# Kernel optimization log

Hardware: AMD Instinct MI355X
Metric: run time of the kernel (lower is better)

Reference implementation:

```python
import jax, jax.numpy as jnp
import numpy as np

B, D, K, L, V = 4096, 512, 10, 256, 80


def setup_inputs() -> dict:
    key = jax.random.key(0)
    k1, k2, k3, k4, k5, k6 = jax.random.split(key, 6)
    inputs = jax.random.normal(k1, (B, D), dtype=jnp.float32)
    prev_kappa = jax.random.uniform(k2, (B, K), dtype=jnp.float32)
    char_ids = jax.random.randint(k3, (B, L), 0, V)
    char_seq_one_hot = jax.nn.one_hot(char_ids, V, dtype=jnp.float32)
    sequence_lengths = jax.random.randint(k4, (B,), 1, L + 1).astype(jnp.int32)
    # Dense params: VarianceScaling(scale=2.0, fan_avg) ~ N(0, 2/((D+3K)/2)) truncated
    std = np.sqrt(2.0 / ((D + 3 * K) / 2.0))
    W = (jax.random.truncated_normal(k5, -2.0, 2.0, (D, 3 * K)) * std).astype(jnp.float32)
    b = jnp.zeros((3 * K,), dtype=jnp.float32)
    kappa_scale = jnp.float32(-2.5)
    return {
        "inputs": inputs,
        "prev_kappa": prev_kappa,
        "char_seq_one_hot": char_seq_one_hot,
        "sequence_lengths": sequence_lengths,
        "W": W,
        "b": b,
        "kappa_scale": kappa_scale,
    }


def reference(inputs, prev_kappa, char_seq_one_hot, sequence_lengths, W, b, kappa_scale):
    raw = inputs @ W + b  # [B, 3K]
    alpha_hat, beta_hat, kappa_hat = jnp.split(raw, 3, axis=1)  # each [B, K]
    alpha = jnp.exp(jnp.clip(alpha_hat, -8.0, 8.0))
    beta = jnp.exp(jnp.clip(beta_hat, -8.0, 8.0))
    delta_kappa = jnp.exp(jnp.clip(kappa_hat + kappa_scale, -8.0, 5.0))
    kappa = prev_kappa + delta_kappa  # [B, K]

    char_len = char_seq_one_hot.shape[1]
    u = jnp.arange(1, char_len + 1, dtype=jnp.float32)  # [L]
    # exponent: [B, K, L]
    exponent = -beta[:, :, None] * jnp.square(kappa[:, :, None] - u[None, None, :])
    exponent = jnp.clip(exponent, -50.0, 0.0)
    phi = jnp.sum(alpha[:, :, None] * jnp.exp(exponent), axis=1)  # [B, L]

    seq_mask = (jnp.arange(char_len)[None, :] < sequence_lengths[:, None]).astype(jnp.float32)
    phi = phi * seq_mask
    phi = jnp.where(jnp.isfinite(phi), phi, 0.0)

    w = jnp.einsum("bl,blv->bv", phi, char_seq_one_hot)  # [B, V]
    w = jnp.where(jnp.isfinite(w), w, 0.0)
    return (w, kappa)
```

## Files before the change

kernel.cpp:

```cpp
#include <hip/hip_runtime.h>

#define B_ 4096
#define D_ 512
#define K_ 10
#define L_ 256
#define V_ 80

__global__ __launch_bounds__(256) void gemv_kernel(
    const float* __restrict__ x,
    const float* __restrict__ prev_kappa,
    const float* __restrict__ W,
    const float* __restrict__ bias,
    const float* __restrict__ kscale,
    float* __restrict__ ws_alpha,
    float* __restrict__ ws_beta,
    float* __restrict__ out_kappa)
{
    const int tid  = threadIdx.x;
    const int wave = tid >> 6;
    const int lane = tid & 63;
    const int r0   = blockIdx.x * 4;
    const int jbase = wave * 8;
    const int jcnt  = (wave == 3) ? 6 : 8;

    const float* xb = x + (size_t)r0 * D_;

    float acc[4][8];
#pragma unroll
    for (int r = 0; r < 4; ++r)
#pragma unroll
        for (int jj = 0; jj < 8; ++jj) acc[r][jj] = 0.f;

#pragma unroll
    for (int i = 0; i < 8; ++i) {
        const int d = lane + 64 * i;
        const float* wrow = W + d * 30 + jbase;
        float wv[8];
#pragma unroll
        for (int jj = 0; jj < 8; ++jj)
            wv[jj] = (jj < 6 || wave < 3) ? wrow[jj] : 0.f;
#pragma unroll
        for (int r = 0; r < 4; ++r) {
            const float xv = xb[r * D_ + d];
#pragma unroll
            for (int jj = 0; jj < 8; ++jj)
                acc[r][jj] = fmaf(xv, wv[jj], acc[r][jj]);
        }
    }

#pragma unroll
    for (int r = 0; r < 4; ++r)
#pragma unroll
        for (int jj = 0; jj < 8; ++jj)
#pragma unroll
            for (int s = 32; s >= 1; s >>= 1)
                acc[r][jj] += __shfl_xor(acc[r][jj], s, 64);

    __shared__ float s_raw[4][30];
    if (lane < jcnt) {
#pragma unroll
        for (int r = 0; r < 4; ++r) {
            float v = acc[r][0];
#pragma unroll
            for (int jj = 1; jj < 8; ++jj) v = (lane == jj) ? acc[r][jj] : v;
            s_raw[r][jbase + lane] = v;
        }
    }
    __syncthreads();

    if (tid < 40) {
        const int r = tid / 10;
        const int k = tid - r * 10;
        const int row = r0 + r;

        const float a_hat = s_raw[r][k]      + bias[k];
        const float b_hat = s_raw[r][10 + k] + bias[10 + k];
        const float k_hat = s_raw[r][20 + k] + bias[20 + k];

        ws_alpha[row * K_ + k] = __expf(fminf(fmaxf(a_hat, -8.f), 8.f));
        ws_beta[row * K_ + k]  = __expf(fminf(fmaxf(b_hat, -8.f), 8.f));
        const float dk = __expf(fminf(fmaxf(k_hat + kscale[0], -8.f), 5.f));
        out_kappa[row * K_ + k] = prev_kappa[row * K_ + k] + dk;
    }
}

__global__ __launch_bounds__(256) void scatter_kernel(
    const float* __restrict__ oh,
    const int*   __restrict__ seqlen,
    const float* __restrict__ ws_alpha,
    const float* __restrict__ ws_beta,
    const float* __restrict__ kappa,
    float* __restrict__ out_w)
{
    const int b   = blockIdx.x;
    const int tid = threadIdx.x;

    __shared__ float s_a[K_], s_b[K_], s_k[K_];
    __shared__ float s_phi[L_];
    __shared__ float s_w[V_];

    if (tid < K_) {
        s_a[tid] = ws_alpha[b * K_ + tid];
        s_b[tid] = ws_beta[b * K_ + tid];
        s_k[tid] = kappa[b * K_ + tid];
    }
    if (tid < V_) s_w[tid] = 0.f;

    const int sl = seqlen[b];
    __syncthreads();

    if (tid < sl) {
        const float u = (float)(tid + 1);
        float phi = 0.f;
#pragma unroll
        for (int k = 0; k < K_; ++k) {
            const float diff = s_k[k] - u;
            float e = fmaxf(-s_b[k] * diff * diff, -50.f);
            phi = fmaf(s_a[k], __expf(e), phi);
        }
        s_phi[tid] = phi;
    }
    __syncthreads();

    const int total4 = sl * (V_ / 4);
    const float4* ohb = (const float4*)(oh + (size_t)b * (L_ * V_));

    for (int f = tid; f < total4; f += 512) {
        const float4 v0 = ohb[f];
        const int f1 = f + 256;
        const bool has1 = (f1 < total4);
        float4 v1 = make_float4(0.f, 0.f, 0.f, 0.f);
        if (has1) v1 = ohb[f1];

        {
            const int l  = f / 20;
            const int vb = (f - l * 20) * 4;
            const float p = s_phi[l];
            if (v0.x != 0.f) atomicAdd(&s_w[vb + 0], p * v0.x);
            if (v0.y != 0.f) atomicAdd(&s_w[vb + 1], p * v0.y);
            if (v0.z != 0.f) atomicAdd(&s_w[vb + 2], p * v0.z);
            if (v0.w != 0.f) atomicAdd(&s_w[vb + 3], p * v0.w);
        }
        if (has1) {
            const int l  = f1 / 20;
            const int vb = (f1 - l * 20) * 4;
            const float p = s_phi[l];
            if (v1.x != 0.f) atomicAdd(&s_w[vb + 0], p * v1.x);
            if (v1.y != 0.f) atomicAdd(&s_w[vb + 1], p * v1.y);
            if (v1.z != 0.f) atomicAdd(&s_w[vb + 2], p * v1.z);
            if (v1.w != 0.f) atomicAdd(&s_w[vb + 3], p * v1.w);
        }
    }
    __syncthreads();

    if (tid < V_) out_w[b * V_ + tid] = s_w[tid];
}

extern "C" void kernel_launch(void* const* d_in, const int* in_sizes, int n_in,
                              void* d_out, int out_size, void* d_ws, size_t ws_size,
                              hipStream_t stream) {
    const float* x          = (const float*)d_in[0];
    const float* prev_kappa = (const float*)d_in[1];
    const float* oh         = (const float*)d_in[2];
    const int*   seqlen     = (const int*)d_in[3];
    const float* W          = (const float*)d_in[4];
    const float* bias       = (const float*)d_in[5];
    const float* kscale     = (const float*)d_in[6];

    float* out   = (float*)d_out;
    float* out_w = out;
    float* out_k = out + B_ * V_;

    float* wsf      = (float*)d_ws;
    float* ws_alpha = wsf;
    float* ws_beta  = wsf + B_ * K_;

    gemv_kernel<<<B_ / 4, 256, 0, stream>>>(x, prev_kappa, W, bias, kscale,
                                            ws_alpha, ws_beta, out_k);
    scatter_kernel<<<B_, 256, 0, stream>>>(oh, seqlen, ws_alpha, ws_beta, out_k,
                                           out_w);
}
```

Baseline: 434.9 us.

## Restructure GEMV via LDS-staged rows and replace atomic scatter with per-column dot reduction

The GEMV kernel now stages 8 input rows in padded shared memory and has each of 240 threads compute one output column with a serial 512-long dot product, replacing the wave-shuffle reduction. The scatter kernel drops shared-memory atomics over float4 one-hot chunks. Instead, 320 threads each own one vocabulary column and one of four row groups, accumulate phi*onehot with strided scalar loads up to a padded sequence length, then reduce the four partials. This removes atomic contention and branchy per-element work, at the cost of uncoalesced-stride reads within a row group and a serial inner loop in the GEMV.

```diff
diff --git a/kernel.cpp b/kernel.cpp
--- a/kernel.cpp
+++ b/kernel.cpp
@@ -5,6 +5,8 @@
 #define K_ 10
 #define L_ 256
 #define V_ 80
+
+#define XSTRIDE 520
 
 __global__ __launch_bounds__(256) void gemv_kernel(
     const float* __restrict__ x,
@@ -16,75 +18,54 @@
     float* __restrict__ ws_beta,
     float* __restrict__ out_kappa)
 {
-    const int tid  = threadIdx.x;
-    const int wave = tid >> 6;
-    const int lane = tid & 63;
-    const int r0   = blockIdx.x * 4;
-    const int jbase = wave * 8;
-    const int jcnt  = (wave == 3) ? 6 : 8;
+    const int tid = threadIdx.x;
+    const int r0  = blockIdx.x * 8;
 
-    const float* xb = x + (size_t)r0 * D_;
+    __shared__ float x_lds[8 * XSTRIDE];
 
-    float acc[4][8];
+    {
+        const float4* xg = (const float4*)(x + (size_t)r0 * D_);
 #pragma unroll
-    for (int r = 0; r < 4; ++r)
-#pragma unroll
-        for (int jj = 0; jj < 8; ++jj) acc[r][jj] = 0.f;
-
-#pragma unroll
-    for (int i = 0; i < 8; ++i) {
-        const int d = lane + 64 * i;
-        const float* wrow = W + d * 30 + jbase;
-        float wv[8];
-#pragma unroll
-        for (int jj = 0; jj < 8; ++jj)
-            wv[jj] = (jj < 6 || wave < 3) ? wrow[jj] : 0.f;
-#pragma unroll
-        for (int r = 0; r < 4; ++r) {
-            const float xv = xb[r * D_ + d];
-#pragma unroll
-            for (int jj = 0; jj < 8; ++jj)
-                acc[r][jj] = fmaf(xv, wv[jj], acc[r][jj]);
-        }
-    }
-
-#pragma unroll
-    for (int r = 0; r < 4; ++r)
-#pragma unroll
-        for (int jj = 0; jj < 8; ++jj)
-#pragma unroll
-            for (int s = 32; s >= 1; s >>= 1)
-                acc[r][jj] += __shfl_xor(acc[r][jj], s, 64);
-
-    __shared__ float s_raw[4][30];
-    if (lane < jcnt) {
-#pragma unroll
-        for (int r = 0; r < 4; ++r) {
-            float v = acc[r][0];
-#pragma unroll
-            for (int jj = 1; jj < 8; ++jj) v = (lane == jj) ? acc[r][jj] : v;
-            s_raw[r][jbase + lane] = v;
+        for (int i = 0; i < 4; ++i) {
+            const int f4 = tid + i * 256;
+            const float4 v = xg[f4];
+            const int f = f4 * 4;
+            const int r = f >> 9;
+            const int c = f & 511;
+            *(float4*)&x_lds[r * XSTRIDE + c] = v;
         }
     }
     __syncthreads();
 
-    if (tid < 40) {
-        const int r = tid / 10;
-        const int k = tid - r * 10;
+    if (tid < 240) {
+        const int r = tid / 30;
+        const int j = tid - r * 30;
         const int row = r0 + r;
+        const float* xr = &x_lds[r * XSTRIDE];
 
-        const float a_hat = s_raw[r][k]      + bias[k];
-        const float b_hat = s_raw[r][10 + k] + bias[10 + k];
-        const float k_hat = s_raw[r][20 + k] + bias[20 + k];
+        float a0 = 0.f, a1 = 0.f, a2 = 0.f, a3 = 0.f;
+#pragma unroll 4
+        for (int d = 0; d < D_; d += 4) {
+            a0 = fmaf(xr[d + 0], W[(d + 0) * 30 + j], a0);
+            a1 = fmaf(xr[d + 1], W[(d + 1) * 30 + j], a1);
+            a2 = fmaf(xr[d + 2], W[(d + 2) * 30 + j], a2);
+            a3 = fmaf(xr[d + 3], W[(d + 3) * 30 + j], a3);
+        }
+        const float v = (a0 + a1) + (a2 + a3) + bias[j];
 
-        ws_alpha[row * K_ + k] = __expf(fminf(fmaxf(a_hat, -8.f), 8.f));
-        ws_beta[row * K_ + k]  = __expf(fminf(fmaxf(b_hat, -8.f), 8.f));
-        const float dk = __expf(fminf(fmaxf(k_hat + kscale[0], -8.f), 5.f));
-        out_kappa[row * K_ + k] = prev_kappa[row * K_ + k] + dk;
+        if (j < 10) {
+            ws_alpha[row * K_ + j] = __expf(fminf(fmaxf(v, -8.f), 8.f));
+        } else if (j < 20) {
+            ws_beta[row * K_ + (j - 10)] = __expf(fminf(fmaxf(v, -8.f), 8.f));
+        } else {
+            const int k = j - 20;
+            const float dk = __expf(fminf(fmaxf(v + kscale[0], -8.f), 5.f));
+            out_kappa[row * K_ + k] = prev_kappa[row * K_ + k] + dk;
+        }
     }
 }
 
-__global__ __launch_bounds__(256) void scatter_kernel(
+__global__ __launch_bounds__(320) void scatter_kernel(
     const float* __restrict__ oh,
     const int*   __restrict__ seqlen,
     const float* __restrict__ ws_alpha,
@@ -97,63 +78,50 @@
 
     __shared__ float s_a[K_], s_b[K_], s_k[K_];
     __shared__ float s_phi[L_];
-    __shared__ float s_w[V_];
+    __shared__ float s_wpart[4 * V_];
 
     if (tid < K_) {
         s_a[tid] = ws_alpha[b * K_ + tid];
         s_b[tid] = ws_beta[b * K_ + tid];
         s_k[tid] = kappa[b * K_ + tid];
     }
-    if (tid < V_) s_w[tid] = 0.f;
-
-    const int sl = seqlen[b];
+    const int sl  = seqlen[b];
+    const int slp = (sl + 15) & ~15;
     __syncthreads();
 
-    if (tid < sl) {
-        const float u = (float)(tid + 1);
+    if (tid < L_) {
         float phi = 0.f;
+        if (tid < sl) {
+            const float u = (float)(tid + 1);
 #pragma unroll
-        for (int k = 0; k < K_; ++k) {
-            const float diff = s_k[k] - u;
-            float e = fmaxf(-s_b[k] * diff * diff, -50.f);
-            phi = fmaf(s_a[k], __expf(e), phi);
+            for (int k = 0; k < K_; ++k) {
+                const float diff = s_k[k] - u;
+                const float e = fmaxf(-s_b[k] * diff * diff, -50.f);
+                phi = fmaf(s_a[k], __expf(e), phi);
+            }
         }
         s_phi[tid] = phi;
     }
     __syncthreads();
 
-    const int total4 = sl * (V_ / 4);
-    const float4* ohb = (const float4*)(oh + (size_t)b * (L_ * V_));
+    const int g = tid / 80;
+    const int v = tid - g * 80;
+    const float* ohb = oh + (size_t)b * (L_ * V_) + v;
 
-    for (int f = tid; f < total4; f += 512) {
-        const float4 v0 = ohb[f];
-        const int f1 = f + 256;
-        const bool has1 = (f1 < total4);
-        float4 v1 = make_float4(0.f, 0.f, 0.f, 0.f);
-        if (has1) v1 = ohb[f1];
-
-        {
-            const int l  = f / 20;
-            const int vb = (f - l * 20) * 4;
-            const float p = s_phi[l];
-            if (v0.x != 0.f) atomicAdd(&s_w[vb + 0], p * v0.x);
-            if (v0.y != 0.f) atomicAdd(&s_w[vb + 1], p * v0.y);
-            if (v0.z != 0.f) atomicAdd(&s_w[vb + 2], p * v0.z);
-            if (v0.w != 0.f) atomicAdd(&s_w[vb + 3], p * v0.w);
-        }
-        if (has1) {
-            const int l  = f1 / 20;
-            const int vb = (f1 - l * 20) * 4;
-            const float p = s_phi[l];
-            if (v1.x != 0.f) atomicAdd(&s_w[vb + 0], p * v1.x);
-            if (v1.y != 0.f) atomicAdd(&s_w[vb + 1], p * v1.y);
-            if (v1.z != 0.f) atomicAdd(&s_w[vb + 2], p * v1.z);
-            if (v1.w != 0.f) atomicAdd(&s_w[vb + 3], p * v1.w);
-        }
+    float a0 = 0.f, a1 = 0.f, a2 = 0.f, a3 = 0.f;
+    for (int l = g; l < slp; l += 16) {
+        a0 = fmaf(s_phi[l],      ohb[(l)      * V_], a0);
+        a1 = fmaf(s_phi[l + 4],  ohb[(l + 4)  * V_], a1);
+        a2 = fmaf(s_phi[l + 8],  ohb[(l + 8)  * V_], a2);
+        a3 = fmaf(s_phi[l + 12], ohb[(l + 12) * V_], a3);
     }
+    s_wpart[g * V_ + v] = (a0 + a1) + (a2 + a3);
     __syncthreads();
 
-    if (tid < V_) out_w[b * V_ + tid] = s_w[tid];
+    if (tid < V_) {
+        out_w[b * V_ + tid] = s_wpart[tid] + s_wpart[V_ + tid] +
+                              s_wpart[2 * V_ + tid] + s_wpart[3 * V_ + tid];
+    }
 }
 
 extern "C" void kernel_launch(void* const* d_in, const int* in_sizes, int n_in,
@@ -175,8 +143,8 @@
     float* ws_alpha = wsf;
     float* ws_beta  = wsf + B_ * K_;
 
-    gemv_kernel<<<B_ / 4, 256, 0, stream>>>(x, prev_kappa, W, bias, kscale,
+    gemv_kernel<<<B_ / 8, 256, 0, stream>>>(x, prev_kappa, W, bias, kscale,
                                             ws_alpha, ws_beta, out_k);
-    scatter_kernel<<<B_, 256, 0, stream>>>(oh, seqlen, ws_alpha, ws_beta, out_k,
+    scatter_kernel<<<B_, 320, 0, stream>>>(oh, seqlen, ws_alpha, ws_beta, out_k,
                                            out_w);
 }
```

Measured after the change: 440.9 us. No clear change (+1.4%).
